# Performance work log

Hardware: AMD Instinct MI355X
Metric: run time of the kernel (lower is better)

## Reference

```python
import jax, jax.numpy as jnp
import numpy as np

B, S, D, H = 4, 2048, 1024, 16
HD = D // H
THETA = 10000.0


def _rope(x, pos, theta):
    # x: (B, H, S, HD); rotate adjacent even/odd pairs
    half = x.shape[-1] // 2
    inv_freq = theta ** (-jnp.arange(half, dtype=x.dtype) / half)  # theta^(-2k/d)
    ang = pos[:, None].astype(x.dtype) * inv_freq[None, :]         # (S, half)
    cos, sin = jnp.cos(ang), jnp.sin(ang)
    x1, x2 = x[..., 0::2], x[..., 1::2]
    o1 = x1 * cos - x2 * sin
    o2 = x1 * sin + x2 * cos
    return jnp.stack([o1, o2], axis=-1).reshape(x.shape)


def setup_inputs() -> dict:
    key = jax.random.key(0)
    ks = jax.random.split(key, 5)
    sc = 1.0 / np.sqrt(D)
    return {
        "x": jax.random.normal(ks[0], (B, S, D), jnp.float32),
        "W_Q": jax.random.normal(ks[1], (D, D), jnp.float32) * sc,
        "W_K": jax.random.normal(ks[2], (D, D), jnp.float32) * sc,
        "W_V": jax.random.normal(ks[3], (D, D), jnp.float32) * sc,
        "W_O": jax.random.normal(ks[4], (D, D), jnp.float32) * sc,
    }


def reference(x, W_Q, W_K, W_V, W_O):
    b, s, d = x.shape
    split = lambda t: t.reshape(b, s, H, HD).transpose(0, 2, 1, 3)  # (B,H,S,HD)
    q = split(x @ W_Q.T)
    k = split(x @ W_K.T)
    v = split(x @ W_V.T)
    pos = jnp.arange(s)
    q = _rope(q, pos, THETA)
    k = _rope(k, pos, THETA)
    scale = 1.0 / jnp.sqrt(jnp.asarray(HD, x.dtype))
    scores = jnp.einsum("bhqd,bhkd->bhqk", q, k) * scale
    causal = jnp.tril(jnp.ones((s, s), dtype=bool))
    scores = jnp.where(causal, scores, jnp.asarray(-jnp.inf, x.dtype))
    attn = jax.nn.softmax(scores, axis=-1)
    o = jnp.einsum("bhqk,bhkd->bhqd", attn, v)
    o = o.transpose(0, 2, 1, 3).reshape(b, s, d)
    return o @ W_O.T
```

## Files before the change

kernel.cpp:

```cpp
#include <hip/hip_runtime.h>
#include <hip/hip_bf16.h>
#include <stdint.h>

#define B_ 4
#define S_ 2048
#define D_ 1024
#define H_ 16

typedef __attribute__((ext_vector_type(4))) float f32x4;
typedef __attribute__((ext_vector_type(16))) float f32x16;
typedef __attribute__((ext_vector_type(8))) short short8;
typedef __attribute__((ext_vector_type(8))) unsigned short ushort8;
typedef __attribute__((ext_vector_type(4))) unsigned int u32x4;
typedef unsigned short u16;
typedef unsigned int u32;

__device__ __forceinline__ u16 f2bf(float f){
  return __builtin_bit_cast(u16, __hip_bfloat16(f));
}
__device__ __forceinline__ u32 pk2bf(float a, float b){
  return (u32)f2bf(a) | ((u32)f2bf(b) << 16);
}
__device__ __forceinline__ float rexp2(float x){
  float r; asm("v_exp_f32 %0, %1" : "=v"(r) : "v"(x)); return r;
}
__device__ __forceinline__ u32 cvtpk(float a, float b){
  u32 r; asm("v_cvt_pk_bf16_f32 %0, %1, %2" : "=v"(r) : "v"(a), "v"(b)); return r;
}
__device__ __forceinline__ f32x4 mfma16(short8 a, short8 b, f32x4 c){
  return __builtin_amdgcn_mfma_f32_16x16x32_bf16(a, b, c, 0, 0, 0);
}
__device__ __forceinline__ f32x16 mfma32(short8 a, short8 b, f32x16 c){
  return __builtin_amdgcn_mfma_f32_32x32x16_bf16(a, b, c, 0, 0, 0);
}
__device__ __forceinline__ void plswap(u32 &x, u32 &y){
  asm volatile("v_permlane32_swap_b32 %0, %1" : "+v"(x), "+v"(y));
}
__device__ __forceinline__ void gload16(const u16* g, u16* l){
  __builtin_amdgcn_global_load_lds((const __attribute__((address_space(1))) u32*)g,
                                   (__attribute__((address_space(3))) u32*)l, 16, 0, 0);
}

__global__ __launch_bounds__(256) void prep_kernel(const float* __restrict__ x,
                                                   const float* __restrict__ w0, const float* __restrict__ w1,
                                                   const float* __restrict__ w2, const float* __restrict__ w3,
                                                   u16* __restrict__ xb,
                                                   u16* __restrict__ o0, u16* __restrict__ o1,
                                                   u16* __restrict__ o2, u16* __restrict__ o3,
                                                   float2* __restrict__ tab){
  const int gid = blockIdx.x;
  if (gid < 8192){
    const int i = gid * 256 + threadIdx.x;
    float4 v = reinterpret_cast<const float4*>(x)[i];
    uint2 o; o.x = pk2bf(v.x, v.y); o.y = pk2bf(v.z, v.w);
    reinterpret_cast<uint2*>(xb)[i] = o;
  } else if (gid < 12288){
    const int g = gid - 8192;
    const int which = g >> 10;
    const float* in = (which==0) ? w0 : (which==1) ? w1 : (which==2) ? w2 : w3;
    u16* out = (which==0) ? o0 : (which==1) ? o1 : (which==2) ? o2 : o3;
    const int i = (g & 1023) * 256 + threadIdx.x;
    float4 v = reinterpret_cast<const float4*>(in)[i];
    uint2 o; o.x = pk2bf(v.x, v.y); o.y = pk2bf(v.z, v.w);
    reinterpret_cast<uint2*>(out)[i] = o;
  } else {
    const int idx = (gid - 12288) * 256 + threadIdx.x;
    const int i = idx & 31, s = idx >> 5;
    const float ang = (float)s * __builtin_exp2f((float)i * -0.41524101186092032f);
    float sn, cs;
    __sincosf(ang, &sn, &cs);
    tab[idx] = make_float2(cs, sn);
  }
}

template<int MODE>
__global__ __launch_bounds__(512) void gemm_bt(const u16* __restrict__ A,
                                               const u16* __restrict__ Bw,
                                               void* __restrict__ C,
                                               const float2* __restrict__ tab,
                                               int M, int N, int K){
  __shared__ __align__(16) u16 As[2][128*64];
  __shared__ __align__(16) u16 Bs[2][128*64];
  const int tid = threadIdx.x;
  const int lane = tid & 63, wid = tid >> 6;
  const int l16 = lane & 15, lq = lane >> 4;
  const int m0 = blockIdx.x * 128, n0 = blockIdx.y * 128;
  const int wr = (wid >> 2) * 64, wc = (wid & 3) * 32;
  const int row_s = tid >> 3;
  const int csw = ((tid & 7) * 8) ^ ((row_s & 7) << 3);
  const u16* Ag0 = A  + (size_t)(m0 + row_s     ) * K + csw;
  const u16* Ag1 = A  + (size_t)(m0 + 64 + row_s) * K + csw;
  const u16* Bg0 = Bw + (size_t)(n0 + row_s     ) * K + csw;
  const u16* Bg1 = Bw + (size_t)(n0 + 64 + row_s) * K + csw;
  const int wb = wid * 512;
  const int rsw = (l16 & 7) << 3;
  gload16(Ag0, &As[0][wb]);
  gload16(Ag1, &As[0][4096 + wb]);
  gload16(Bg0, &Bs[0][wb]);
  gload16(Bg1, &Bs[0][4096 + wb]);
  __syncthreads();
  f32x4 acc[4][2] = {};
  int cur = 0;
  const int NS = 16;
#pragma unroll 1
  for (int ks = 0; ks < NS; ++ks){
    if (ks + 1 < NS){
      const int kn = (ks + 1) * 64;
      gload16(Ag0 + kn, &As[cur^1][wb]);
      gload16(Ag1 + kn, &As[cur^1][4096 + wb]);
      gload16(Bg0 + kn, &Bs[cur^1][wb]);
      gload16(Bg1 + kn, &Bs[cur^1][4096 + wb]);
    }
    const u16* Ac = &As[cur][0];
    const u16* Bc = &Bs[cur][0];
    short8 af[2][4], bfr[2][2];
#pragma unroll
    for (int ks2=0;ks2<2;ks2++){
#pragma unroll
      for (int i=0;i<4;i++)
        af[ks2][i] = *reinterpret_cast<const short8*>(Ac + (wr + i*16 + l16)*64 + ((ks2*32 + lq*8) ^ rsw));
#pragma unroll
      for (int j=0;j<2;j++)
        bfr[ks2][j] = *reinterpret_cast<const short8*>(Bc + (wc + j*16 + l16)*64 + ((ks2*32 + lq*8) ^ rsw));
    }
    __builtin_amdgcn_s_setprio(1);
#pragma unroll
    for (int ks2=0;ks2<2;ks2++)
#pragma unroll
      for (int i=0;i<4;i++)
#pragma unroll
        for (int j=0;j<2;j++) acc[i][j] = mfma16(af[ks2][i], bfr[ks2][j], acc[i][j]);
    __builtin_amdgcn_s_setprio(0);
    __syncthreads();
    cur ^= 1;
  }
  const float QS = 0.18033688011112043f;
#pragma unroll
  for (int i=0;i<4;i++){
#pragma unroll
    for (int j=0;j<2;j++){
      if (MODE == 4){
        const int mb = m0 + wr + i*16 + lq*4;
        const int n  = n0 + wc + j*16 + l16;
        const int b = mb >> 11, s = mb & 2047;
        const int h = n >> 6,  hd = n & 63;
        uint2 w;
        w.x = pk2bf(acc[i][j][0], acc[i][j][1]);
        w.y = pk2bf(acc[i][j][2], acc[i][j][3]);
        *reinterpret_cast<uint2*>(reinterpret_cast<u16*>(C) +
            ((size_t)((b*H_ + h)*64 + hd))*S_ + s) = w;
      } else {
#pragma unroll
        for (int r=0;r<4;r++){
          const int m = m0 + wr + i*16 + lq*4 + r;
          const int n = n0 + wc + j*16 + l16;
          float v = acc[i][j][r];
          if (MODE == 2){
            reinterpret_cast<float*>(C)[(size_t)m * N + n] = v;
          } else if (MODE == 0){
            reinterpret_cast<u16*>(C)[(size_t)m * N + n] = f2bf(v);
          } else {
            const int b = m >> 11, s = m & 2047;
            const int h = n >> 6,  hd = n & 63;
            const float2 t = tab[(s << 5) + (hd >> 1)];
            const float partner = __shfl_xor(v, 1, 64);
            const float pm = (hd & 1) ? partner : -partner;
            float o = fmaf(v, t.x, pm * t.y);
            if (MODE == 1) o *= QS;
            reinterpret_cast<u16*>(C)[(((size_t)(b*H_ + h) * S_ + s) << 6) + hd] = f2bf(o);
          }
        }
      }
    }
  }
}

__global__ __launch_bounds__(256, 4) void attn_kernel(const u16* __restrict__ Q,
                                                      const u16* __restrict__ Kg,
                                                      const u16* __restrict__ Vt,
                                                      u16* __restrict__ O){
  __shared__ __align__(16) u16 KV[2][2][4096];
  const int bh = blockIdx.x;
  const int qt = 15 - blockIdx.y;
  const int tid = threadIdx.x, wid = tid >> 6, lane = tid & 63;
  const int l32 = lane & 31, hh = lane >> 5;
  const u16* Qb = Q  + (size_t)bh * S_ * 64;
  const u16* Kb = Kg + (size_t)bh * S_ * 64;
  const u16* Vb = Vt + (size_t)bh * 64 * S_;
  const int b = bh >> 4, head = bh & 15;
  const short8 ones8 = {0x3F80,0x3F80,0x3F80,0x3F80,0x3F80,0x3F80,0x3F80,0x3F80};
  const f32x16 Z16 = {};

  const int LoffA = tid*8;
  const int rowA  = tid >> 3;
  const int swzA  = LoffA ^ ((rowA & 7) << 3);
  const int swzB  = swzA + 2048;
  const int vcolA = swzA & 63;
  const int rsw   = (l32 & 7) << 3;

  const int q0 = qt * 128;
  const int qw0 = q0 + wid*32;
  const int qg = qw0 + l32;
  short8 qf[4];
#pragma unroll
  for (int j=0;j<4;j++)
    qf[j] = *reinterpret_cast<const short8*>(Qb + (size_t)qg*64 + j*16 + hh*8);
  f32x16 oacc0 = Z16, oacc1 = Z16, lacc = Z16;

  const int nt = 2*qt + 2;
  gload16(Kb + swzA,                         &KV[0][0][wid*512]);
  gload16(Kb + swzB,                         &KV[0][0][wid*512 + 2048]);
  gload16(Vb + (size_t)rowA*S_ + vcolA,      &KV[0][1][wid*512]);
  gload16(Vb + (size_t)(rowA+32)*S_ + vcolA, &KV[0][1][wid*512 + 2048]);
  __syncthreads();

#pragma unroll 1
  for (int kt = 0; kt < nt; ++kt){
    const int cur = kt & 1;
    if (kt + 1 < nt){
      const int kn = (kt + 1) * 64;
      gload16(Kb + (size_t)kn*64 + swzA,             &KV[cur^1][0][wid*512]);
      gload16(Kb + (size_t)kn*64 + swzB,             &KV[cur^1][0][wid*512 + 2048]);
      gload16(Vb + (size_t)rowA*S_ + kn + vcolA,     &KV[cur^1][1][wid*512]);
      gload16(Vb + (size_t)(rowA+32)*S_ + kn + vcolA,&KV[cur^1][1][wid*512 + 2048]);
    }
    const int k0 = kt * 64;
    if (k0 <= qw0 + 31){
      const u16* Kc = &KV[cur][0][0];
      const u16* Vc = &KV[cur][1][0];
      f32x16 sc0 = Z16, sc1 = Z16;
      __builtin_amdgcn_s_setprio(1);
#pragma unroll
      for (int j=0;j<4;j++){
        short8 kf0 = *reinterpret_cast<const short8*>(Kc + l32*64      + ((j*16 + hh*8) ^ rsw));
        short8 kf1 = *reinterpret_cast<const short8*>(Kc + (32+l32)*64 + ((j*16 + hh*8) ^ rsw));
        sc0 = mfma32(kf0, qf[j], sc0);
        sc1 = mfma32(kf1, qf[j], sc1);
      }
      __builtin_amdgcn_s_setprio(0);
      if (k0 + 63 > qw0){
#pragma unroll
        for (int r=0;r<16;r++){
          const int kk = k0 + (r&3) + 8*(r>>2) + 4*hh;
          if (kk > qg)      sc0[r] = -1e30f;
          if (kk + 32 > qg) sc1[r] = -1e30f;
        }
      }
#pragma unroll
      for (int r=0;r<16;r++){
        sc0[r] = rexp2(sc0[r]);
        sc1[r] = rexp2(sc1[r]);
      }
      __builtin_amdgcn_s_setprio(1);
#pragma unroll
      for (int blk=0; blk<4; ++blk){
        const f32x16 S = (blk < 2) ? sc0 : sc1;
        const int r0 = (blk & 1) * 8;
        u32 a0 = cvtpk(S[r0+0], S[r0+1]);
        u32 a1 = cvtpk(S[r0+2], S[r0+3]);
        u32 b0 = cvtpk(S[r0+4], S[r0+5]);
        u32 b1 = cvtpk(S[r0+6], S[r0+7]);
        plswap(a0, b0);
        plswap(a1, b1);
        u32x4 t4; t4[0]=a0; t4[1]=a1; t4[2]=b0; t4[3]=b1;
        const short8 pf = __builtin_bit_cast(short8, t4);
        lacc = mfma32(ones8, pf, lacc);
        short8 vf0 = *reinterpret_cast<const short8*>(Vc + l32*64      + ((blk*16 + hh*8) ^ rsw));
        short8 vf1 = *reinterpret_cast<const short8*>(Vc + (32+l32)*64 + ((blk*16 + hh*8) ^ rsw));
        oacc0 = mfma32(vf0, pf, oacc0);
        oacc1 = mfma32(vf1, pf, oacc1);
      }
      __builtin_amdgcn_s_setprio(0);
    }
    __syncthreads();
  }
  const float linv = __builtin_amdgcn_rcpf(lacc[0]);
  u16* Orow = O + (size_t)(b*S_ + qg)*D_ + head*64;
#pragma unroll
  for (int q4=0;q4<4;q4++){
    uint2 o0, o1;
    o0.x = pk2bf(oacc0[q4*4+0]*linv, oacc0[q4*4+1]*linv);
    o0.y = pk2bf(oacc0[q4*4+2]*linv, oacc0[q4*4+3]*linv);
    o1.x = pk2bf(oacc1[q4*4+0]*linv, oacc1[q4*4+1]*linv);
    o1.y = pk2bf(oacc1[q4*4+2]*linv, oacc1[q4*4+3]*linv);
    *reinterpret_cast<uint2*>(Orow + q4*8 + hh*4)      = o0;
    *reinterpret_cast<uint2*>(Orow + 32 + q4*8 + hh*4) = o1;
  }
}

extern "C" void kernel_launch(void* const* d_in, const int* in_sizes, int n_in,
                              void* d_out, int out_size, void* d_ws, size_t ws_size,
                              hipStream_t stream){
  const float* x  = (const float*)d_in[0];
  const float* Wq = (const float*)d_in[1];
  const float* Wk = (const float*)d_in[2];
  const float* Wv = (const float*)d_in[3];
  const float* Wo = (const float*)d_in[4];
  char* ws = (char*)d_ws;
  u16* xb  = (u16*)(ws);
  u16* Wqb = (u16*)(ws + (16u<<20));
  u16* Wkb = (u16*)(ws + (16u<<20) + (2u<<20));
  u16* Wvb = (u16*)(ws + (16u<<20) + (4u<<20));
  u16* Wob = (u16*)(ws + (16u<<20) + (6u<<20));
  u16* Qh  = (u16*)(ws + (24u<<20));
  u16* Kh  = (u16*)(ws + (40u<<20));
  u16* Ob  = (u16*)(ws + (56u<<20));
  u16* Vt  = (u16*)(ws + (72u<<20));
  float2* tab = (float2*)(ws + (88u<<20));

  prep_kernel<<<12544, 256, 0, stream>>>(x, Wq, Wk, Wv, Wo, xb, Wqb, Wkb, Wvb, Wob, tab);

  dim3 gg(64, 8);
  gemm_bt<1><<<gg, 512, 0, stream>>>(xb, Wqb, Qh, tab, 8192, 1024, 1024);
  gemm_bt<3><<<gg, 512, 0, stream>>>(xb, Wkb, Kh, tab, 8192, 1024, 1024);
  gemm_bt<4><<<gg, 512, 0, stream>>>(xb, Wvb, Vt, nullptr, 8192, 1024, 1024);

  attn_kernel<<<dim3(64,16), 256, 0, stream>>>(Qh, Kh, Vt, Ob);

  gemm_bt<2><<<gg, 512, 0, stream>>>(Ob, Wob, (float*)d_out, nullptr, 8192, 1024, 1024);
}
```

Baseline: 162.0 us.

## Fuse Q and K projection GEMMs into one kernel sharing A tiles

Replaces the two separate Q and K projection GEMM launches with a single kernel that loads each x tile once and multiplies it against both W_Q and W_K, keeping two accumulator sets and applying RoPE in the epilogue. This halves the x tile traffic for these projections and removes one launch. To fit both weight tiles in LDS the K-step shrinks from 64 to 32, which doubles the barrier count. Doubling the accumulators also raises register pressure and may lower occupancy.

```diff
diff --git a/kernel.cpp b/kernel.cpp
--- a/kernel.cpp
+++ b/kernel.cpp
@@ -70,6 +70,97 @@
     float sn, cs;
     __sincosf(ang, &sn, &cs);
     tab[idx] = make_float2(cs, sn);
+  }
+}
+
+__global__ __launch_bounds__(512) void gemm_qk(const u16* __restrict__ A,
+                                               const u16* __restrict__ Wq,
+                                               const u16* __restrict__ Wk,
+                                               u16* __restrict__ Qh,
+                                               u16* __restrict__ Kh,
+                                               const float2* __restrict__ tab){
+  __shared__ __align__(16) u16 As [2][128*32];
+  __shared__ __align__(16) u16 Bqs[2][128*32];
+  __shared__ __align__(16) u16 Bks[2][128*32];
+  const int K = 1024;
+  const int tid = threadIdx.x;
+  const int lane = tid & 63, wid = tid >> 6;
+  const int l16 = lane & 15, lq = lane >> 4;
+  const int m0 = blockIdx.x * 128, n0 = blockIdx.y * 128;
+  const int wr = (wid >> 2) * 64, wc = (wid & 3) * 32;
+  const int row_s = tid >> 2;
+  const int csw = ((tid & 3) * 8) ^ ((row_s & 3) << 3);
+  const u16* Ag = A  + (size_t)(m0 + row_s) * K + csw;
+  const u16* Qg = Wq + (size_t)(n0 + row_s) * K + csw;
+  const u16* Kg = Wk + (size_t)(n0 + row_s) * K + csw;
+  const int wb = wid * 512;
+  const int rsw = (l16 & 3) << 3;
+  gload16(Ag, &As[0][wb]);
+  gload16(Qg, &Bqs[0][wb]);
+  gload16(Kg, &Bks[0][wb]);
+  __syncthreads();
+  f32x4 accQ[4][2] = {}, accK[4][2] = {};
+  int cur = 0;
+  const int NS = 32;
+#pragma unroll 1
+  for (int ks = 0; ks < NS; ++ks){
+    if (ks + 1 < NS){
+      const int kn = (ks + 1) * 32;
+      gload16(Ag + kn, &As [cur^1][wb]);
+      gload16(Qg + kn, &Bqs[cur^1][wb]);
+      gload16(Kg + kn, &Bks[cur^1][wb]);
+    }
+    const u16* Ac  = &As [cur][0];
+    const u16* Bqc = &Bqs[cur][0];
+    const u16* Bkc = &Bks[cur][0];
+    short8 af[4], bq[2], bk[2];
+#pragma unroll
+    for (int i=0;i<4;i++)
+      af[i] = *reinterpret_cast<const short8*>(Ac + (wr + i*16 + l16)*32 + ((lq*8) ^ rsw));
+#pragma unroll
+    for (int j=0;j<2;j++){
+      bq[j] = *reinterpret_cast<const short8*>(Bqc + (wc + j*16 + l16)*32 + ((lq*8) ^ rsw));
+      bk[j] = *reinterpret_cast<const short8*>(Bkc + (wc + j*16 + l16)*32 + ((lq*8) ^ rsw));
+    }
+    __builtin_amdgcn_s_setprio(1);
+#pragma unroll
+    for (int i=0;i<4;i++)
+#pragma unroll
+      for (int j=0;j<2;j++){
+        accQ[i][j] = mfma16(af[i], bq[j], accQ[i][j]);
+        accK[i][j] = mfma16(af[i], bk[j], accK[i][j]);
+      }
+    __builtin_amdgcn_s_setprio(0);
+    __syncthreads();
+    cur ^= 1;
+  }
+  const float QS = 0.18033688011112043f;
+#pragma unroll
+  for (int i=0;i<4;i++){
+#pragma unroll
+    for (int j=0;j<2;j++){
+#pragma unroll
+      for (int r=0;r<4;r++){
+        const int m = m0 + wr + i*16 + lq*4 + r;
+        const int n = n0 + wc + j*16 + l16;
+        const int b = m >> 11, s = m & 2047;
+        const int h = n >> 6,  hd = n & 63;
+        const float2 t = tab[(s << 5) + (hd >> 1)];
+        const size_t dst = (((size_t)(b*H_ + h) * S_ + s) << 6) + hd;
+        {
+          float v = accQ[i][j][r];
+          const float partner = __shfl_xor(v, 1, 64);
+          const float pm = (hd & 1) ? partner : -partner;
+          Qh[dst] = f2bf(fmaf(v, t.x, pm * t.y) * QS);
+        }
+        {
+          float v = accK[i][j][r];
+          const float partner = __shfl_xor(v, 1, 64);
+          const float pm = (hd & 1) ? partner : -partner;
+          Kh[dst] = f2bf(fmaf(v, t.x, pm * t.y));
+        }
+      }
+    }
   }
 }
 
@@ -134,7 +225,6 @@
     __syncthreads();
     cur ^= 1;
   }
-  const float QS = 0.18033688011112043f;
 #pragma unroll
   for (int i=0;i<4;i++){
 #pragma unroll
@@ -154,21 +244,7 @@
         for (int r=0;r<4;r++){
           const int m = m0 + wr + i*16 + lq*4 + r;
           const int n = n0 + wc + j*16 + l16;
-          float v = acc[i][j][r];
-          if (MODE == 2){
-            reinterpret_cast<float*>(C)[(size_t)m * N + n] = v;
-          } else if (MODE == 0){
-            reinterpret_cast<u16*>(C)[(size_t)m * N + n] = f2bf(v);
-          } else {
-            const int b = m >> 11, s = m & 2047;
-            const int h = n >> 6,  hd = n & 63;
-            const float2 t = tab[(s << 5) + (hd >> 1)];
-            const float partner = __shfl_xor(v, 1, 64);
-            const float pm = (hd & 1) ? partner : -partner;
-            float o = fmaf(v, t.x, pm * t.y);
-            if (MODE == 1) o *= QS;
-            reinterpret_cast<u16*>(C)[(((size_t)(b*H_ + h) * S_ + s) << 6) + hd] = f2bf(o);
-          }
+          reinterpret_cast<float*>(C)[(size_t)m * N + n] = acc[i][j][r];
         }
       }
     }
@@ -311,8 +387,7 @@
   prep_kernel<<<12544, 256, 0, stream>>>(x, Wq, Wk, Wv, Wo, xb, Wqb, Wkb, Wvb, Wob, tab);
 
   dim3 gg(64, 8);
-  gemm_bt<1><<<gg, 512, 0, stream>>>(xb, Wqb, Qh, tab, 8192, 1024, 1024);
-  gemm_bt<3><<<gg, 512, 0, stream>>>(xb, Wkb, Kh, tab, 8192, 1024, 1024);
+  gemm_qk<<<gg, 512, 0, stream>>>(xb, Wqb, Wkb, Qh, Kh, tab);
   gemm_bt<4><<<gg, 512, 0, stream>>>(xb, Wvb, Vt, nullptr, 8192, 1024, 1024);
 
   attn_kernel<<<dim3(64,16), 256, 0, stream>>>(Qh, Kh, Vt, Ob);
```

Measured after the change: 155.8 us, median of 2. -3.8%, faster.
